# Optimization experiments

Measured on AMD Instinct MI355X. Metric: run time of the kernel, lower is better.

## Reference

```python
import jax, jax.numpy as jnp
import numpy as np

N_ITER = 3
EPS = 1e-8


def _squash(v):
    # v: [B, 1, D]; norm over last (feature) dim
    norm = jnp.linalg.norm(v, axis=2, keepdims=True)
    scale = norm ** 2 / (1 + norm ** 2) / (norm + EPS)
    return scale * v


def setup_inputs() -> dict:
    key = jax.random.key(0)
    k1, k2 = jax.random.split(key)
    B, N, D = 64, 4096, 256
    x = jax.random.normal(k1, (B, N, D), dtype=jnp.float32)
    m = jax.random.uniform(k2, (B, N, 1), dtype=jnp.float32)
    return {"x": x, "m": m}


def reference(x, m):
    # x: [B, N, D], m: [B, N, 1]
    x = m * x
    B, N, _ = x.shape
    b = jnp.zeros((B, N, 1), dtype=x.dtype)
    s = None
    for _ in range(N_ITER):
        w = jax.nn.softmax(m * b, axis=1)            # [B, N, 1]
        sigma = jnp.sum(w * x, axis=1, keepdims=True)  # [B, 1, D]  (== bmm(w^T, x))
        s = _squash(sigma)                            # [B, 1, D]
        b_new = jnp.sum(s * x, axis=2, keepdims=True)  # [B, N, 1]
        b = b + b_new
    w = jax.nn.softmax(b, axis=1)                     # [B, N, 1]
    s = s.reshape(s.shape[0], s.shape[-1])            # [B, D]
    w = w.reshape(w.shape[0], w.shape[1])             # [B, N]
    return (w, s)
```

## Files before the change

### kernel.cpp

```cpp
#include <hip/hip_runtime.h>
#include <math.h>

#define BB 64
#define NN 4096
#define DD 256

template<bool FINAL>
__global__ __launch_bounds__(256) void fpass_kernel(
    const float* __restrict__ x, const float* __restrict__ m,
    const float* __restrict__ s_buf, float* __restrict__ b_buf,
    float* __restrict__ part_sig, float* __restrict__ part_M,
    float* __restrict__ part_Z, int P, int rowsPerWave)
{
    const int lane = threadIdx.x & 63;
    const int wib  = threadIdx.x >> 6;
    const int bpb  = P >> 2;
    const int batch = blockIdx.x / bpb;
    const int p = (blockIdx.x % bpb) * 4 + wib;
    const int n0 = p * rowsPerWave;

    const float4 s4 = reinterpret_cast<const float4*>(s_buf + batch * DD)[lane];
    const float4* __restrict__ xr =
        reinterpret_cast<const float4*>(x + ((size_t)batch * NN + n0) * DD) + lane;
    const float* __restrict__ mrow = m + (size_t)batch * NN + n0;
    float* __restrict__ brow = b_buf + (size_t)batch * NN + n0;

    float M = -INFINITY, Z = 0.f;
    float sx = 0.f, sy = 0.f, sz = 0.f, sw = 0.f;

    auto upd = [&](float bn, float mn, const float4& xv) {
        float l = FINAL ? bn : mn * bn;
        float newM = fmaxf(M, l);
        float c = __expf(M - newM);
        float e = __expf(l - newM);
        Z = Z * c + e;
        if (!FINAL) {
            float wgt = e * mn;
            sx = sx * c + wgt * xv.x;
            sy = sy * c + wgt * xv.y;
            sz = sz * c + wgt * xv.z;
            sw = sw * c + wgt * xv.w;
        }
        M = newM;
    };

    for (int r0 = 0; r0 < rowsPerWave; r0 += 4) {
        float4 xv0 = xr[(size_t)(r0 + 0) * (DD / 4)];
        float4 xv1 = xr[(size_t)(r0 + 1) * (DD / 4)];
        float4 xv2 = xr[(size_t)(r0 + 2) * (DD / 4)];
        float4 xv3 = xr[(size_t)(r0 + 3) * (DD / 4)];
        const float4 m4 = *reinterpret_cast<const float4*>(mrow + r0);
        const float4 b4 = *reinterpret_cast<const float4*>(brow + r0);

        float dp0 = xv0.x * s4.x + xv0.y * s4.y + xv0.z * s4.z + xv0.w * s4.w;
        float dp1 = xv1.x * s4.x + xv1.y * s4.y + xv1.z * s4.z + xv1.w * s4.w;
        float dp2 = xv2.x * s4.x + xv2.y * s4.y + xv2.z * s4.z + xv2.w * s4.w;
        float dp3 = xv3.x * s4.x + xv3.y * s4.y + xv3.z * s4.z + xv3.w * s4.w;
        #pragma unroll
        for (int off = 32; off; off >>= 1) {
            dp0 += __shfl_xor(dp0, off, 64);
            dp1 += __shfl_xor(dp1, off, 64);
            dp2 += __shfl_xor(dp2, off, 64);
            dp3 += __shfl_xor(dp3, off, 64);
        }
        float bn0 = b4.x + m4.x * dp0;
        float bn1 = b4.y + m4.y * dp1;
        float bn2 = b4.z + m4.z * dp2;
        float bn3 = b4.w + m4.w * dp3;
        if (lane == 0)
            *reinterpret_cast<float4*>(brow + r0) = make_float4(bn0, bn1, bn2, bn3);
        upd(bn0, m4.x, xv0);
        upd(bn1, m4.y, xv1);
        upd(bn2, m4.z, xv2);
        upd(bn3, m4.w, xv3);
    }
    if (!FINAL) {
        reinterpret_cast<float4*>(part_sig + ((size_t)batch * P + p) * DD)[lane] =
            make_float4(sx, sy, sz, sw);
    }
    if (lane == 0) {
        part_M[batch * P + p] = M;
        part_Z[batch * P + p] = Z;
    }
}

template<bool FINAL>
__global__ __launch_bounds__(1024) void reduce_kernel(
    const float* __restrict__ part_sig, const float* __restrict__ part_M,
    const float* __restrict__ part_Z, float* __restrict__ s_buf,
    float* __restrict__ s_out, float* __restrict__ MZf, int P)
{
    const int b = blockIdx.x;
    const int tid = threadIdx.x;
    __shared__ float red[1024];
    __shared__ float csh[128];
    __shared__ float mg_sh, zg_sh;

    if (tid < 64) {
        float M0 = (tid < P) ? part_M[b * P + tid] : -INFINITY;
        float M1 = (tid + 64 < P) ? part_M[b * P + tid + 64] : -INFINITY;
        float Mm = fmaxf(M0, M1);
        #pragma unroll
        for (int off = 32; off; off >>= 1) Mm = fmaxf(Mm, __shfl_xor(Mm, off, 64));
        float c0 = (tid < P) ? expf(M0 - Mm) : 0.f;
        float c1 = (tid + 64 < P) ? expf(M1 - Mm) : 0.f;
        if (tid < P) csh[tid] = c0;
        if (tid + 64 < P) csh[tid + 64] = c1;
        float Zs = ((tid < P) ? part_Z[b * P + tid] : 0.f) * c0
                 + ((tid + 64 < P) ? part_Z[b * P + tid + 64] : 0.f) * c1;
        #pragma unroll
        for (int off = 32; off; off >>= 1) Zs += __shfl_xor(Zs, off, 64);
        if (tid == 0) { mg_sh = Mm; zg_sh = Zs; }
    }
    __syncthreads();

    if (FINAL) {
        if (tid == 0) { MZf[2 * b] = mg_sh; MZf[2 * b + 1] = zg_sh; }
        return;
    }

    const int q = tid >> 8;
    const int d = tid & 255;
    float sig = 0.f;
    #pragma unroll 4
    for (int k = q; k < P; k += 4)
        sig += csh[k] * part_sig[((size_t)b * P + k) * DD + d];
    red[tid] = sig;
    __syncthreads();

    if (tid < 256) {
        sig = red[tid] + red[tid + 256] + red[tid + 512] + red[tid + 768];
        sig /= zg_sh;
        red[tid] = sig * sig;
    }
    __syncthreads();
    for (int s = 128; s > 0; s >>= 1) {
        if (tid < s) red[tid] += red[tid + s];
        __syncthreads();
    }
    if (tid < 256) {
        float n2 = red[0];
        float nrm = sqrtf(n2);
        float scale = n2 / (1.f + n2) / (nrm + 1e-8f);
        float sv = scale * sig;
        s_buf[b * DD + tid] = sv;
        if (s_out) s_out[b * DD + tid] = sv;
    }
}

__global__ __launch_bounds__(256) void w_kernel(
    const float* __restrict__ b_buf, const float* __restrict__ MZf,
    float* __restrict__ w_out)
{
    int i = blockIdx.x * 256 + threadIdx.x;
    int b = i >> 10;
    float Mg = MZf[2 * b];
    float iZ = 1.f / MZf[2 * b + 1];
    float4 bv = reinterpret_cast<const float4*>(b_buf)[i];
    float4 wv;
    wv.x = __expf(bv.x - Mg) * iZ;
    wv.y = __expf(bv.y - Mg) * iZ;
    wv.z = __expf(bv.z - Mg) * iZ;
    wv.w = __expf(bv.w - Mg) * iZ;
    reinterpret_cast<float4*>(w_out)[i] = wv;
}

extern "C" void kernel_launch(void* const* d_in, const int* in_sizes, int n_in,
                              void* d_out, int out_size, void* d_ws, size_t ws_size,
                              hipStream_t stream)
{
    const float* x = (const float*)d_in[0];
    const float* m = (const float*)d_in[1];
    float* out = (float*)d_out;

    int P = 128;
    auto needBytes = [](int Pv) -> size_t {
        return (size_t)(BB * NN + BB * DD + (size_t)BB * Pv * DD + BB * Pv * 2 + 2 * BB)
               * sizeof(float);
    };
    while (P > 8 && needBytes(P) > ws_size) P >>= 1;

    float* ws       = (float*)d_ws;
    float* b_buf    = ws;
    float* s_buf    = b_buf + BB * NN;
    float* part_sig = s_buf + BB * DD;
    float* part_M   = part_sig + (size_t)BB * P * DD;
    float* part_Z   = part_M + BB * P;
    float* MZf      = part_Z + BB * P;

    hipMemsetAsync(ws, 0, (size_t)(BB * NN + BB * DD) * sizeof(float), stream);

    const int rpw = NN / P;
    const int blocksF = BB * P / 4;
    float* s_final = out + BB * NN;

    for (int it = 0; it < 3; ++it) {
        fpass_kernel<false><<<blocksF, 256, 0, stream>>>(
            x, m, s_buf, b_buf, part_sig, part_M, part_Z, P, rpw);
        reduce_kernel<false><<<BB, 1024, 0, stream>>>(
            part_sig, part_M, part_Z, s_buf, (it == 2) ? s_final : nullptr, MZf, P);
    }
    fpass_kernel<true><<<blocksF, 256, 0, stream>>>(
        x, m, s_buf, b_buf, part_sig, part_M, part_Z, P, rpw);
    reduce_kernel<true><<<BB, 1024, 0, stream>>>(
        part_sig, part_M, part_Z, s_buf, nullptr, MZf, P);
    w_kernel<<<BB * NN / 1024, 256, 0, stream>>>(b_buf, MZf, out);
}
```

Baseline: 514.3 us.

## Cache m-scaled x in fp16 workspace and specialise first routing pass

A new first pass exploits b=0 (uniform softmax) to compute sigma as a plain sum of m*x, and writes m*x as fp16 into the workspace. Later passes read the half-size fp16 copy instead of fp32 x, which halves the main memory traffic for three of the four sweeps. This costs an extra 128MB write in the first pass. Rounding the activations to fp16 may shift results against the fp32 reference.

```diff
diff --git a/kernel.cpp b/kernel.cpp
--- a/kernel.cpp
+++ b/kernel.cpp
@@ -5,12 +5,14 @@
 #define NN 4096
 #define DD 256
 
-template<bool FINAL>
-__global__ __launch_bounds__(256) void fpass_kernel(
+typedef _Float16 f16;
+typedef f16 f16x4 __attribute__((ext_vector_type(4)));
+
+__global__ __launch_bounds__(256) void pass1_kernel(
     const float* __restrict__ x, const float* __restrict__ m,
-    const float* __restrict__ s_buf, float* __restrict__ b_buf,
-    float* __restrict__ part_sig, float* __restrict__ part_M,
-    float* __restrict__ part_Z, int P, int rowsPerWave)
+    f16* __restrict__ xt, float* __restrict__ part_sig,
+    float* __restrict__ part_M, float* __restrict__ part_Z,
+    int P, int rowsPerWave)
 {
     const int lane = threadIdx.x & 63;
     const int wib  = threadIdx.x >> 6;
@@ -19,9 +21,61 @@
     const int p = (blockIdx.x % bpb) * 4 + wib;
     const int n0 = p * rowsPerWave;
 
-    const float4 s4 = reinterpret_cast<const float4*>(s_buf + batch * DD)[lane];
     const float4* __restrict__ xr =
         reinterpret_cast<const float4*>(x + ((size_t)batch * NN + n0) * DD) + lane;
+    f16x4* __restrict__ xtr =
+        reinterpret_cast<f16x4*>(xt + ((size_t)batch * NN + n0) * DD) + lane;
+    const float* __restrict__ mrow = m + (size_t)batch * NN + n0;
+
+    float sx = 0.f, sy = 0.f, sz = 0.f, sw = 0.f;
+
+    for (int r0 = 0; r0 < rowsPerWave; r0 += 4) {
+        float4 xv0 = xr[(size_t)(r0 + 0) * (DD / 4)];
+        float4 xv1 = xr[(size_t)(r0 + 1) * (DD / 4)];
+        float4 xv2 = xr[(size_t)(r0 + 2) * (DD / 4)];
+        float4 xv3 = xr[(size_t)(r0 + 3) * (DD / 4)];
+        const float4 m4 = *reinterpret_cast<const float4*>(mrow + r0);
+
+        float4 t0 = make_float4(m4.x * xv0.x, m4.x * xv0.y, m4.x * xv0.z, m4.x * xv0.w);
+        float4 t1 = make_float4(m4.y * xv1.x, m4.y * xv1.y, m4.y * xv1.z, m4.y * xv1.w);
+        float4 t2 = make_float4(m4.z * xv2.x, m4.z * xv2.y, m4.z * xv2.z, m4.z * xv2.w);
+        float4 t3 = make_float4(m4.w * xv3.x, m4.w * xv3.y, m4.w * xv3.z, m4.w * xv3.w);
+
+        xtr[(size_t)(r0 + 0) * (DD / 4)] = f16x4{(f16)t0.x, (f16)t0.y, (f16)t0.z, (f16)t0.w};
+        xtr[(size_t)(r0 + 1) * (DD / 4)] = f16x4{(f16)t1.x, (f16)t1.y, (f16)t1.z, (f16)t1.w};
+        xtr[(size_t)(r0 + 2) * (DD / 4)] = f16x4{(f16)t2.x, (f16)t2.y, (f16)t2.z, (f16)t2.w};
+        xtr[(size_t)(r0 + 3) * (DD / 4)] = f16x4{(f16)t3.x, (f16)t3.y, (f16)t3.z, (f16)t3.w};
+
+        sx += t0.x + t1.x + t2.x + t3.x;
+        sy += t0.y + t1.y + t2.y + t3.y;
+        sz += t0.z + t1.z + t2.z + t3.z;
+        sw += t0.w + t1.w + t2.w + t3.w;
+    }
+    reinterpret_cast<float4*>(part_sig + ((size_t)batch * P + p) * DD)[lane] =
+        make_float4(sx, sy, sz, sw);
+    if (lane == 0) {
+        part_M[batch * P + p] = 0.f;
+        part_Z[batch * P + p] = (float)rowsPerWave;
+    }
+}
+
+template<bool FINAL>
+__global__ __launch_bounds__(256) void fpass16_kernel(
+    const f16* __restrict__ xt, const float* __restrict__ m,
+    const float* __restrict__ s_buf, float* __restrict__ b_buf,
+    float* __restrict__ part_sig, float* __restrict__ part_M,
+    float* __restrict__ part_Z, int P, int rowsPerWave)
+{
+    const int lane = threadIdx.x & 63;
+    const int wib  = threadIdx.x >> 6;
+    const int bpb  = P >> 2;
+    const int batch = blockIdx.x / bpb;
+    const int p = (blockIdx.x % bpb) * 4 + wib;
+    const int n0 = p * rowsPerWave;
+
+    const float4 s4 = reinterpret_cast<const float4*>(s_buf + batch * DD)[lane];
+    const f16x4* __restrict__ xr =
+        reinterpret_cast<const f16x4*>(xt + ((size_t)batch * NN + n0) * DD) + lane;
     const float* __restrict__ mrow = m + (size_t)batch * NN + n0;
     float* __restrict__ brow = b_buf + (size_t)batch * NN + n0;
 
@@ -35,22 +89,26 @@
         float e = __expf(l - newM);
         Z = Z * c + e;
         if (!FINAL) {
-            float wgt = e * mn;
-            sx = sx * c + wgt * xv.x;
-            sy = sy * c + wgt * xv.y;
-            sz = sz * c + wgt * xv.z;
-            sw = sw * c + wgt * xv.w;
+            sx = sx * c + e * xv.x;
+            sy = sy * c + e * xv.y;
+            sz = sz * c + e * xv.z;
+            sw = sw * c + e * xv.w;
         }
         M = newM;
     };
 
     for (int r0 = 0; r0 < rowsPerWave; r0 += 4) {
-        float4 xv0 = xr[(size_t)(r0 + 0) * (DD / 4)];
-        float4 xv1 = xr[(size_t)(r0 + 1) * (DD / 4)];
-        float4 xv2 = xr[(size_t)(r0 + 2) * (DD / 4)];
-        float4 xv3 = xr[(size_t)(r0 + 3) * (DD / 4)];
+        f16x4 h0 = xr[(size_t)(r0 + 0) * (DD / 4)];
+        f16x4 h1 = xr[(size_t)(r0 + 1) * (DD / 4)];
+        f16x4 h2 = xr[(size_t)(r0 + 2) * (DD / 4)];
+        f16x4 h3 = xr[(size_t)(r0 + 3) * (DD / 4)];
         const float4 m4 = *reinterpret_cast<const float4*>(mrow + r0);
         const float4 b4 = *reinterpret_cast<const float4*>(brow + r0);
+
+        float4 xv0 = make_float4((float)h0.x, (float)h0.y, (float)h0.z, (float)h0.w);
+        float4 xv1 = make_float4((float)h1.x, (float)h1.y, (float)h1.z, (float)h1.w);
+        float4 xv2 = make_float4((float)h2.x, (float)h2.y, (float)h2.z, (float)h2.w);
+        float4 xv3 = make_float4((float)h3.x, (float)h3.y, (float)h3.z, (float)h3.w);
 
         float dp0 = xv0.x * s4.x + xv0.y * s4.y + xv0.z * s4.z + xv0.w * s4.w;
         float dp1 = xv1.x * s4.x + xv1.y * s4.y + xv1.z * s4.z + xv1.w * s4.w;
@@ -63,10 +121,10 @@
             dp2 += __shfl_xor(dp2, off, 64);
             dp3 += __shfl_xor(dp3, off, 64);
         }
-        float bn0 = b4.x + m4.x * dp0;
-        float bn1 = b4.y + m4.y * dp1;
-        float bn2 = b4.z + m4.z * dp2;
-        float bn3 = b4.w + m4.w * dp3;
+        float bn0 = b4.x + dp0;
+        float bn1 = b4.y + dp1;
+        float bn2 = b4.z + dp2;
+        float bn3 = b4.w + dp3;
         if (lane == 0)
             *reinterpret_cast<float4*>(brow + r0) = make_float4(bn0, bn1, bn2, bn3);
         upd(bn0, m4.x, xv0);
@@ -173,35 +231,42 @@
     const float* m = (const float*)d_in[1];
     float* out = (float*)d_out;
 
+    const size_t xtElems = (size_t)BB * NN * DD;
     int P = 128;
-    auto needBytes = [](int Pv) -> size_t {
-        return (size_t)(BB * NN + BB * DD + (size_t)BB * Pv * DD + BB * Pv * 2 + 2 * BB)
+    auto needBytes = [&](int Pv) -> size_t {
+        return xtElems * sizeof(f16) +
+               (size_t)(BB * NN + BB * DD + (size_t)BB * Pv * DD + BB * Pv * 2 + 2 * BB)
                * sizeof(float);
     };
     while (P > 8 && needBytes(P) > ws_size) P >>= 1;
 
-    float* ws       = (float*)d_ws;
-    float* b_buf    = ws;
+    f16*   xt       = (f16*)d_ws;
+    float* b_buf    = (float*)(xt + xtElems);
     float* s_buf    = b_buf + BB * NN;
     float* part_sig = s_buf + BB * DD;
     float* part_M   = part_sig + (size_t)BB * P * DD;
     float* part_Z   = part_M + BB * P;
     float* MZf      = part_Z + BB * P;
 
-    hipMemsetAsync(ws, 0, (size_t)(BB * NN + BB * DD) * sizeof(float), stream);
+    hipMemsetAsync(b_buf, 0, (size_t)(BB * NN) * sizeof(float), stream);
 
     const int rpw = NN / P;
     const int blocksF = BB * P / 4;
     float* s_final = out + BB * NN;
 
-    for (int it = 0; it < 3; ++it) {
-        fpass_kernel<false><<<blocksF, 256, 0, stream>>>(
-            x, m, s_buf, b_buf, part_sig, part_M, part_Z, P, rpw);
+    pass1_kernel<<<blocksF, 256, 0, stream>>>(
+        x, m, xt, part_sig, part_M, part_Z, P, rpw);
+    reduce_kernel<false><<<BB, 1024, 0, stream>>>(
+        part_sig, part_M, part_Z, s_buf, nullptr, MZf, P);
+
+    for (int it = 1; it < 3; ++it) {
+        fpass16_kernel<false><<<blocksF, 256, 0, stream>>>(
+            xt, m, s_buf, b_buf, part_sig, part_M, part_Z, P, rpw);
         reduce_kernel<false><<<BB, 1024, 0, stream>>>(
             part_sig, part_M, part_Z, s_buf, (it == 2) ? s_final : nullptr, MZf, P);
     }
-    fpass_kernel<true><<<blocksF, 256, 0, stream>>>(
-        x, m, s_buf, b_buf, part_sig, part_M, part_Z, P, rpw);
+    fpass16_kernel<true><<<blocksF, 256, 0, stream>>>(
+        xt, m, s_buf, b_buf, part_sig, part_M, part_Z, P, rpw);
     reduce_kernel<true><<<BB, 1024, 0, stream>>>(
         part_sig, part_M, part_Z, s_buf, nullptr, MZf, P);
     w_kernel<<<BB * NN / 1024, 256, 0, stream>>>(b_buf, MZf, out);
```

New measurement: 480.4 us. 1.07x faster.
